# Performance work log

Hardware: AMD Instinct MI355X
Metric: run time of the kernel (lower is better)

## Reference

```python
import jax, jax.numpy as jnp
import numpy as np

N_FEATURES = 128
N_ACTIONS = 16
HIDDEN = 256
BATCH = 4096
IN_DIM = N_FEATURES + N_ACTIONS  # 144


def setup_inputs() -> dict:
    key = jax.random.key(0)
    k1, k2, k3, k4 = jax.random.split(key, 4)
    f_t = jax.random.normal(k1, (BATCH, N_FEATURES), dtype=jnp.float32)
    a_t = jax.random.normal(k2, (BATCH, N_ACTIONS), dtype=jnp.float32)
    # Stacked per-feature MLP params (one small MLP per output feature).
    W1 = jax.random.normal(k3, (N_FEATURES, IN_DIM, HIDDEN), dtype=jnp.float32) / np.sqrt(IN_DIM)
    b1 = jnp.zeros((N_FEATURES, HIDDEN), dtype=jnp.float32)
    W2 = jax.random.normal(k4, (N_FEATURES, HIDDEN), dtype=jnp.float32) / np.sqrt(HIDDEN)
    b2 = jnp.zeros((N_FEATURES,), dtype=jnp.float32)
    return {"f_t": f_t, "a_t": a_t, "W1": W1, "b1": b1, "W2": W2, "b2": b2}


def reference(f_t, a_t, W1, b1, W2, b2):
    # fa_t: [B, F+A] shared input to all per-feature models
    fa_t = jnp.concatenate((f_t, a_t), axis=1)
    # Grouped GEMM replacing parallel_apply over n_features tiny MLPs:
    # h: [M, B, H]
    h = jax.nn.relu(jnp.einsum('bi,mih->mbh', fa_t, W1) + b1[:, None, :])
    # out: [B, M]  (each model emits a single scalar per example)
    out = jnp.einsum('mbh,mh->bm', h, W2) + b2[None, :]
    # skip_connection=True, additional=False, all=False -> add f_t
    return out + f_t
```

## Files before the change

### kernel.cpp

```cpp
#include <hip/hip_runtime.h>
#include <hip/hip_bf16.h>

#define BATCH   4096
#define NF      128
#define NA      16
#define IN_DIM  144
#define KP      144
#define KF      192
#define HID     256

typedef __attribute__((ext_vector_type(8))) short bf16x8;
typedef __attribute__((ext_vector_type(4))) float f32x4;
typedef __attribute__((ext_vector_type(16))) float f32x16;
typedef unsigned int u32;

__device__ __forceinline__ void gl_lds16(const void* gsrc, void* ldst) {
    __builtin_amdgcn_global_load_lds(
        (const __attribute__((address_space(1))) u32*)gsrc,
        (__attribute__((address_space(3))) u32*)ldst, 16, 0, 0);
}

__device__ __host__ __forceinline__ int swzkey(int row) {
    return (row + (row >> 3)) & 7;
}

__global__ void convert_all(const float* __restrict__ W1,
                            const float* __restrict__ f_t,
                            const float* __restrict__ a_t,
                            __hip_bfloat16* __restrict__ w1t,
                            __hip_bfloat16* __restrict__ fab) {
    const int bid = blockIdx.x;
    const int t = threadIdx.x;
    if (bid < 1152) {
        __shared__ float tile[16][HID];
        int m = bid / 9;
        int kc = bid - m * 9;
        int k0 = kc * 16;
#pragma unroll
        for (int i = 0; i < 16; ++i)
            tile[i][t] = W1[((size_t)m * IN_DIM + (k0 + i)) * HID + t];
        __syncthreads();
        union { ushort us[16]; uint4 q[2]; } pk;
#pragma unroll
        for (int i = 0; i < 16; ++i) {
            __hip_bfloat16 h = __float2bfloat16(tile[i][t]);
            pk.us[i] = *(ushort*)&h;
        }
        uint4* dst = (uint4*)(w1t + ((size_t)m * HID + t) * KP + k0);
        dst[0] = pk.q[0];
        dst[1] = pk.q[1];
    } else {
        int c = (bid - 1152) * 256 + t;
        const int total = BATCH * (KF / 8);
        if (c >= total) return;
        int row = c / 24;
        int cc = c - row * 24;
        union { ushort us[8]; uint4 q; } pk;
#pragma unroll
        for (int j = 0; j < 8; ++j) {
            int k = cc * 8 + j;
            float v;
            if (k < NF)            v = f_t[(size_t)row * NF + k];
            else if (k < IN_DIM)   v = a_t[(size_t)row * NA + (k - NF)];
            else                   v = 0.0f;
            __hip_bfloat16 h = __float2bfloat16(v);
            pk.us[j] = *(ushort*)&h;
        }
        int pc = cc ^ swzkey(row);
        *(uint4*)(fab + (size_t)row * KF + pc * 8) = pk.q;
    }
}

__global__ __launch_bounds__(256, 2) void fused_mlp(
        const __hip_bfloat16* __restrict__ fab,
        const __hip_bfloat16* __restrict__ w1t,
        const float* __restrict__ b1,
        const float* __restrict__ W2,
        const float* __restrict__ b2,
        const float* __restrict__ f_t,
        float* __restrict__ out) {
    __shared__ __align__(16) __hip_bfloat16 Abuf[2][64 * KF];
    __shared__ __align__(16) float partial[2][4][64];

    const int bid = blockIdx.x;
    const int m     = bid & 127;
    const int slice = bid >> 7;
    const int row_base = slice * 1024;
    const int t = threadIdx.x;
    const int w = t >> 6;
    const int lane = t & 63;
    const int l31 = lane & 31;
    const int h = lane >> 5;
    const int x0 = swzkey(l31) << 4;
    const int x1 = ((swzkey(l31) + 4) & 7) << 4;

    bf16x8 bfrag[2][9];
#pragma unroll
    for (int hi2 = 0; hi2 < 2; ++hi2) {
        const int col = w * 64 + hi2 * 32 + l31;
        const __hip_bfloat16* wp = w1t + ((size_t)m * HID + col) * KP + h * 8;
#pragma unroll
        for (int ks = 0; ks < 9; ++ks)
            bfrag[hi2][ks] = *(const bf16x8*)(wp + ks * 16);
    }
    f32x16 w2v[2], b1v[2];
#pragma unroll
    for (int hi2 = 0; hi2 < 2; ++hi2) {
        const float* wp2 = W2 + (size_t)m * HID + w * 64 + hi2 * 32 + 4 * h;
        const float* bp1 = b1 + (size_t)m * HID + w * 64 + hi2 * 32 + 4 * h;
#pragma unroll
        for (int q = 0; q < 4; ++q) {
            f32x4 v = *(const f32x4*)(wp2 + 8 * q);
            f32x4 bv = *(const f32x4*)(bp1 + 8 * q);
#pragma unroll
            for (int i = 0; i < 4; ++i) {
                w2v[hi2][q * 4 + i] = v[i];
                b1v[hi2][q * 4 + i] = bv[i];
            }
        }
    }
    const float b2v = b2[m];

    {
        const char* src = (const char*)(fab + (size_t)row_base * KF);
        char* dst = (char*)&Abuf[0][0];
#pragma unroll
        for (int i = 0; i < 6; ++i)
            gl_lds16(src + (size_t)(t + i * 256) * 16, dst + (t + i * 256) * 16);
    }
    __syncthreads();

    for (int tile = 0; tile < 16; ++tile) {
        const int cur = tile & 1;
        const int r0 = row_base + tile * 64;

        if (tile < 15) {
            const char* src = (const char*)(fab + (size_t)(r0 + 64) * KF);
            char* dst = (char*)&Abuf[cur ^ 1][0];
#pragma unroll
            for (int i = 0; i < 6; ++i)
                gl_lds16(src + (size_t)(t + i * 256) * 16, dst + (t + i * 256) * 16);
        }
        float skipv = 0.0f;
        if (t < 64) skipv = f_t[(size_t)(r0 + t) * NF + m];

        f32x16 acc[2][2];
        const char* ab = (const char*)&Abuf[cur][0];

        {
            bf16x8 a[2];
            a[0] = *(const bf16x8*)(ab + l31 * 384 + ((h * 16) ^ x0));
            a[1] = *(const bf16x8*)(ab + (32 + l31) * 384 + ((h * 16) ^ x1));
#pragma unroll
            for (int hi2 = 0; hi2 < 2; ++hi2)
#pragma unroll
                for (int bj2 = 0; bj2 < 2; ++bj2)
                    acc[hi2][bj2] = __builtin_amdgcn_mfma_f32_32x32x16_bf16(
                        bfrag[hi2][0], a[bj2], b1v[hi2], 0, 0, 0);
        }
#pragma unroll
        for (int ks = 1; ks < 9; ++ks) {
            bf16x8 a[2];
            int cb = ks * 32 + h * 16;
            a[0] = *(const bf16x8*)(ab + l31 * 384 + (cb ^ x0));
            a[1] = *(const bf16x8*)(ab + (32 + l31) * 384 + (cb ^ x1));
#pragma unroll
            for (int hi2 = 0; hi2 < 2; ++hi2)
#pragma unroll
                for (int bj2 = 0; bj2 < 2; ++bj2)
                    acc[hi2][bj2] = __builtin_amdgcn_mfma_f32_32x32x16_bf16(
                        bfrag[hi2][ks], a[bj2], acc[hi2][bj2], 0, 0, 0);
        }

        float sarr[2];
#pragma unroll
        for (int bj2 = 0; bj2 < 2; ++bj2) {
            float sr0 = 0.f, sr1 = 0.f, sr2 = 0.f, sr3 = 0.f;
#pragma unroll
            for (int hi2 = 0; hi2 < 2; ++hi2)
#pragma unroll
                for (int q = 0; q < 4; ++q) {
                    float h0 = acc[hi2][bj2][q*4+0]; h0 = h0 > 0.f ? h0 : 0.f;
                    float h1 = acc[hi2][bj2][q*4+1]; h1 = h1 > 0.f ? h1 : 0.f;
                    float h2 = acc[hi2][bj2][q*4+2]; h2 = h2 > 0.f ? h2 : 0.f;
                    float h3 = acc[hi2][bj2][q*4+3]; h3 = h3 > 0.f ? h3 : 0.f;
                    sr0 = fmaf(h0, w2v[hi2][q*4+0], sr0);
                    sr1 = fmaf(h1, w2v[hi2][q*4+1], sr1);
                    sr2 = fmaf(h2, w2v[hi2][q*4+2], sr2);
                    sr3 = fmaf(h3, w2v[hi2][q*4+3], sr3);
                }
            float s = (sr0 + sr1) + (sr2 + sr3);
            s += __shfl_xor(s, 32, 64);
            sarr[bj2] = s;
        }
        if (h == 0) {
            partial[cur][w][l31]      = sarr[0];
            partial[cur][w][32 + l31] = sarr[1];
        }

        __syncthreads();
        if (t < 64) {
            float v = (partial[cur][0][t] + partial[cur][1][t])
                    + (partial[cur][2][t] + partial[cur][3][t])
                    + b2v + skipv;
            out[(size_t)(r0 + t) * NF + m] = v;
        }
    }
}

extern "C" void kernel_launch(void* const* d_in, const int* in_sizes, int n_in,
                              void* d_out, int out_size, void* d_ws, size_t ws_size,
                              hipStream_t stream) {
    const float* f_t = (const float*)d_in[0];
    const float* a_t = (const float*)d_in[1];
    const float* W1  = (const float*)d_in[2];
    const float* b1  = (const float*)d_in[3];
    const float* W2  = (const float*)d_in[4];
    const float* b2  = (const float*)d_in[5];
    float* out = (float*)d_out;

    __hip_bfloat16* w1t = (__hip_bfloat16*)d_ws;
    __hip_bfloat16* fab = (__hip_bfloat16*)((char*)d_ws + (size_t)NF * HID * KP * 2);

    hipLaunchKernelGGL(convert_all, dim3(1536), dim3(256), 0, stream,
                       W1, f_t, a_t, w1t, fab);
    hipLaunchKernelGGL(fused_mlp, dim3(512), dim3(256), 0, stream,
                       fab, w1t, b1, W2, b2, f_t, out);
}
```

Measured before the change: 56.69 us.

## Load activations directly from global in MFMA-fragment layout, drop LDS staging

The activation matrix is now written by the conversion kernel in a chunked layout of 8-element k-chunks by batch row, so each lane can load its MFMA A-fragment directly from global memory. This removes the swizzled LDS double buffer, the global-to-LDS copies and the per-tile __syncthreads. Partial sums for all 16 tiles are kept in LDS and reduced once at the end, with the output writes and skip-add spread across all threads. In exchange, every k-step now waits on global/L2 latency with no explicit prefetch, and the padding in the activation buffer is removed.

```diff
diff --git a/kernel.cpp b/kernel.cpp
--- a/kernel.cpp
+++ b/kernel.cpp
@@ -6,29 +6,18 @@
 #define NA      16
 #define IN_DIM  144
 #define KP      144
-#define KF      192
+#define NKC     18
 #define HID     256
 
 typedef __attribute__((ext_vector_type(8))) short bf16x8;
 typedef __attribute__((ext_vector_type(4))) float f32x4;
 typedef __attribute__((ext_vector_type(16))) float f32x16;
-typedef unsigned int u32;
-
-__device__ __forceinline__ void gl_lds16(const void* gsrc, void* ldst) {
-    __builtin_amdgcn_global_load_lds(
-        (const __attribute__((address_space(1))) u32*)gsrc,
-        (__attribute__((address_space(3))) u32*)ldst, 16, 0, 0);
-}
-
-__device__ __host__ __forceinline__ int swzkey(int row) {
-    return (row + (row >> 3)) & 7;
-}
 
 __global__ void convert_all(const float* __restrict__ W1,
                             const float* __restrict__ f_t,
                             const float* __restrict__ a_t,
                             __hip_bfloat16* __restrict__ w1t,
-                            __hip_bfloat16* __restrict__ fab) {
+                            __hip_bfloat16* __restrict__ fab2) {
     const int bid = blockIdx.x;
     const int t = threadIdx.x;
     if (bid < 1152) {
@@ -50,37 +39,31 @@
         dst[0] = pk.q[0];
         dst[1] = pk.q[1];
     } else {
-        int c = (bid - 1152) * 256 + t;
-        const int total = BATCH * (KF / 8);
-        if (c >= total) return;
-        int row = c / 24;
-        int cc = c - row * 24;
+        int b2i = bid - 1152;
+        int cc = b2i / 16;
+        int rb = b2i - cc * 16;
+        int row = rb * 256 + t;
         union { ushort us[8]; uint4 q; } pk;
+        const float* src = (cc < 16) ? (f_t + (size_t)row * NF + cc * 8)
+                                     : (a_t + (size_t)row * NA + (cc - 16) * 8);
 #pragma unroll
         for (int j = 0; j < 8; ++j) {
-            int k = cc * 8 + j;
-            float v;
-            if (k < NF)            v = f_t[(size_t)row * NF + k];
-            else if (k < IN_DIM)   v = a_t[(size_t)row * NA + (k - NF)];
-            else                   v = 0.0f;
-            __hip_bfloat16 h = __float2bfloat16(v);
+            __hip_bfloat16 h = __float2bfloat16(src[j]);
             pk.us[j] = *(ushort*)&h;
         }
-        int pc = cc ^ swzkey(row);
-        *(uint4*)(fab + (size_t)row * KF + pc * 8) = pk.q;
+        *(uint4*)(fab2 + ((size_t)cc * BATCH + row) * 8) = pk.q;
     }
 }
 
 __global__ __launch_bounds__(256, 2) void fused_mlp(
-        const __hip_bfloat16* __restrict__ fab,
+        const __hip_bfloat16* __restrict__ fab2,
         const __hip_bfloat16* __restrict__ w1t,
         const float* __restrict__ b1,
         const float* __restrict__ W2,
         const float* __restrict__ b2,
         const float* __restrict__ f_t,
         float* __restrict__ out) {
-    __shared__ __align__(16) __hip_bfloat16 Abuf[2][64 * KF];
-    __shared__ __align__(16) float partial[2][4][64];
+    __shared__ __align__(16) float partial[16][4][64];
 
     const int bid = blockIdx.x;
     const int m     = bid & 127;
@@ -91,8 +74,6 @@
     const int lane = t & 63;
     const int l31 = lane & 31;
     const int h = lane >> 5;
-    const int x0 = swzkey(l31) << 4;
-    const int x1 = ((swzkey(l31) + 4) & 7) << 4;
 
     bf16x8 bfrag[2][9];
 #pragma unroll
@@ -121,55 +102,35 @@
     }
     const float b2v = b2[m];
 
-    {
-        const char* src = (const char*)(fab + (size_t)row_base * KF);
-        char* dst = (char*)&Abuf[0][0];
-#pragma unroll
-        for (int i = 0; i < 6; ++i)
-            gl_lds16(src + (size_t)(t + i * 256) * 16, dst + (t + i * 256) * 16);
-    }
-    __syncthreads();
-
     for (int tile = 0; tile < 16; ++tile) {
-        const int cur = tile & 1;
         const int r0 = row_base + tile * 64;
-
-        if (tile < 15) {
-            const char* src = (const char*)(fab + (size_t)(r0 + 64) * KF);
-            char* dst = (char*)&Abuf[cur ^ 1][0];
-#pragma unroll
-            for (int i = 0; i < 6; ++i)
-                gl_lds16(src + (size_t)(t + i * 256) * 16, dst + (t + i * 256) * 16);
-        }
-        float skipv = 0.0f;
-        if (t < 64) skipv = f_t[(size_t)(r0 + t) * NF + m];
+        const __hip_bfloat16* fb0 = fab2 + ((size_t)h * BATCH + r0 + l31) * 8;
+        const __hip_bfloat16* fb1 = fb0 + 32 * 8;
 
         f32x16 acc[2][2];
-        const char* ab = (const char*)&Abuf[cur][0];
 
         {
-            bf16x8 a[2];
-            a[0] = *(const bf16x8*)(ab + l31 * 384 + ((h * 16) ^ x0));
-            a[1] = *(const bf16x8*)(ab + (32 + l31) * 384 + ((h * 16) ^ x1));
+            bf16x8 a0 = *(const bf16x8*)fb0;
+            bf16x8 a1 = *(const bf16x8*)fb1;
 #pragma unroll
-            for (int hi2 = 0; hi2 < 2; ++hi2)
-#pragma unroll
-                for (int bj2 = 0; bj2 < 2; ++bj2)
-                    acc[hi2][bj2] = __builtin_amdgcn_mfma_f32_32x32x16_bf16(
-                        bfrag[hi2][0], a[bj2], b1v[hi2], 0, 0, 0);
+            for (int hi2 = 0; hi2 < 2; ++hi2) {
+                acc[hi2][0] = __builtin_amdgcn_mfma_f32_32x32x16_bf16(
+                    bfrag[hi2][0], a0, b1v[hi2], 0, 0, 0);
+                acc[hi2][1] = __builtin_amdgcn_mfma_f32_32x32x16_bf16(
+                    bfrag[hi2][0], a1, b1v[hi2], 0, 0, 0);
+            }
         }
 #pragma unroll
         for (int ks = 1; ks < 9; ++ks) {
-            bf16x8 a[2];
-            int cb = ks * 32 + h * 16;
-            a[0] = *(const bf16x8*)(ab + l31 * 384 + (cb ^ x0));
-            a[1] = *(const bf16x8*)(ab + (32 + l31) * 384 + (cb ^ x1));
+            bf16x8 a0 = *(const bf16x8*)(fb0 + (size_t)ks * 2 * BATCH * 8);
+            bf16x8 a1 = *(const bf16x8*)(fb1 + (size_t)ks * 2 * BATCH * 8);
 #pragma unroll
-            for (int hi2 = 0; hi2 < 2; ++hi2)
-#pragma unroll
-                for (int bj2 = 0; bj2 < 2; ++bj2)
-                    acc[hi2][bj2] = __builtin_amdgcn_mfma_f32_32x32x16_bf16(
-                        bfrag[hi2][ks], a[bj2], acc[hi2][bj2], 0, 0, 0);
+            for (int hi2 = 0; hi2 < 2; ++hi2) {
+                acc[hi2][0] = __builtin_amdgcn_mfma_f32_32x32x16_bf16(
+                    bfrag[hi2][ks], a0, acc[hi2][0], 0, 0, 0);
+                acc[hi2][1] = __builtin_amdgcn_mfma_f32_32x32x16_bf16(
+                    bfrag[hi2][ks], a1, acc[hi2][1], 0, 0, 0);
+            }
         }
 
         float sarr[2];
@@ -194,17 +155,22 @@
             sarr[bj2] = s;
         }
         if (h == 0) {
-            partial[cur][w][l31]      = sarr[0];
-            partial[cur][w][32 + l31] = sarr[1];
+            partial[tile][w][l31]      = sarr[0];
+            partial[tile][w][32 + l31] = sarr[1];
         }
+    }
 
-        __syncthreads();
-        if (t < 64) {
-            float v = (partial[cur][0][t] + partial[cur][1][t])
-                    + (partial[cur][2][t] + partial[cur][3][t])
-                    + b2v + skipv;
-            out[(size_t)(r0 + t) * NF + m] = v;
-        }
+    __syncthreads();
+#pragma unroll
+    for (int i = 0; i < 4; ++i) {
+        int idx = i * 256 + t;
+        int tl = idx >> 6;
+        int r  = idx & 63;
+        int row = row_base + tl * 64 + r;
+        float v = (partial[tl][0][r] + partial[tl][1][r])
+                + (partial[tl][2][r] + partial[tl][3][r])
+                + b2v + f_t[(size_t)row * NF + m];
+        out[(size_t)row * NF + m] = v;
     }
 }
 
@@ -219,11 +185,11 @@
     const float* b2  = (const float*)d_in[5];
     float* out = (float*)d_out;
 
-    __hip_bfloat16* w1t = (__hip_bfloat16*)d_ws;
-    __hip_bfloat16* fab = (__hip_bfloat16*)((char*)d_ws + (size_t)NF * HID * KP * 2);
+    __hip_bfloat16* w1t  = (__hip_bfloat16*)d_ws;
+    __hip_bfloat16* fab2 = (__hip_bfloat16*)((char*)d_ws + (size_t)NF * HID * KP * 2);
 
-    hipLaunchKernelGGL(convert_all, dim3(1536), dim3(256), 0, stream,
-                       W1, f_t, a_t, w1t, fab);
+    hipLaunchKernelGGL(convert_all, dim3(1440), dim3(256), 0, stream,
+                       W1, f_t, a_t, w1t, fab2);
     hipLaunchKernelGGL(fused_mlp, dim3(512), dim3(256), 0, stream,
-                       fab, w1t, b1, W2, b2, f_t, out);
+                       fab2, w1t, b1, W2, b2, f_t, out);
 }
```

Measured after the change: 59.72 us. +5.3%, slower.

## Store activations chunk-major per tile, drop K padding, and double the grid

Applied to the files above, without the earlier changes.

Activations are now written in a chunk-major layout per 64-row tile (18 chunks of 8 bf16) instead of padded row-major 192-wide rows with an XOR swizzle. This removes the zero-padding to 192 columns and makes LDS fragment reads contiguous without swizzle arithmetic. Each block now handles 512 rows instead of 1024, so the grid doubles to 1024 blocks for better occupancy and load balance. The cost is more redundant loading of per-model weight fragments into registers, since twice as many blocks each load them.

```diff
diff --git a/kernel.cpp b/kernel.cpp
--- a/kernel.cpp
+++ b/kernel.cpp
@@ -6,7 +6,7 @@
 #define NA      16
 #define IN_DIM  144
 #define KP      144
-#define KF      192
+#define NCH     18
 #define HID     256
 
 typedef __attribute__((ext_vector_type(8))) short bf16x8;
@@ -20,15 +20,11 @@
         (__attribute__((address_space(3))) u32*)ldst, 16, 0, 0);
 }
 
-__device__ __host__ __forceinline__ int swzkey(int row) {
-    return (row + (row >> 3)) & 7;
-}
-
 __global__ void convert_all(const float* __restrict__ W1,
                             const float* __restrict__ f_t,
                             const float* __restrict__ a_t,
                             __hip_bfloat16* __restrict__ w1t,
-                            __hip_bfloat16* __restrict__ fab) {
+                            __hip_bfloat16* __restrict__ fabT) {
     const int bid = blockIdx.x;
     const int t = threadIdx.x;
     if (bid < 1152) {
@@ -50,49 +46,46 @@
         dst[0] = pk.q[0];
         dst[1] = pk.q[1];
     } else {
-        int c = (bid - 1152) * 256 + t;
-        const int total = BATCH * (KF / 8);
-        if (c >= total) return;
-        int row = c / 24;
-        int cc = c - row * 24;
+        int o = (bid - 1152) * 256 + t;
+        const int total = (BATCH / 64) * NCH * 64;
+        if (o >= total) return;
+        int r  = o & 63;
+        int cc = (o >> 6) % NCH;
+        int T  = o / (NCH * 64);
+        int row = T * 64 + r;
         union { ushort us[8]; uint4 q; } pk;
+        const float* src = (cc < 16) ? (f_t + (size_t)row * NF + cc * 8)
+                                     : (a_t + (size_t)row * NA + (cc - 16) * 8);
 #pragma unroll
         for (int j = 0; j < 8; ++j) {
-            int k = cc * 8 + j;
-            float v;
-            if (k < NF)            v = f_t[(size_t)row * NF + k];
-            else if (k < IN_DIM)   v = a_t[(size_t)row * NA + (k - NF)];
-            else                   v = 0.0f;
-            __hip_bfloat16 h = __float2bfloat16(v);
+            __hip_bfloat16 h = __float2bfloat16(src[j]);
             pk.us[j] = *(ushort*)&h;
         }
-        int pc = cc ^ swzkey(row);
-        *(uint4*)(fab + (size_t)row * KF + pc * 8) = pk.q;
+        *(uint4*)(fabT + (size_t)o * 8) = pk.q;
     }
 }
 
 __global__ __launch_bounds__(256, 2) void fused_mlp(
-        const __hip_bfloat16* __restrict__ fab,
+        const __hip_bfloat16* __restrict__ fabT,
         const __hip_bfloat16* __restrict__ w1t,
         const float* __restrict__ b1,
         const float* __restrict__ W2,
         const float* __restrict__ b2,
         const float* __restrict__ f_t,
         float* __restrict__ out) {
-    __shared__ __align__(16) __hip_bfloat16 Abuf[2][64 * KF];
+    __shared__ __align__(16) __hip_bfloat16 Abuf[2][NCH * 64 * 8];
     __shared__ __align__(16) float partial[2][4][64];
 
     const int bid = blockIdx.x;
     const int m     = bid & 127;
     const int slice = bid >> 7;
-    const int row_base = slice * 1024;
+    const int row_base = slice * 512;
+    const int T0 = row_base / 64;
     const int t = threadIdx.x;
     const int w = t >> 6;
     const int lane = t & 63;
     const int l31 = lane & 31;
     const int h = lane >> 5;
-    const int x0 = swzkey(l31) << 4;
-    const int x1 = ((swzkey(l31) + 4) & 7) << 4;
 
     bf16x8 bfrag[2][9];
 #pragma unroll
@@ -121,26 +114,27 @@
     }
     const float b2v = b2[m];
 
-    {
-        const char* src = (const char*)(fab + (size_t)row_base * KF);
-        char* dst = (char*)&Abuf[0][0];
-#pragma unroll
-        for (int i = 0; i < 6; ++i)
-            gl_lds16(src + (size_t)(t + i * 256) * 16, dst + (t + i * 256) * 16);
-    }
+#define STAGE(BUF, TG)                                                        \
+    {                                                                         \
+        const char* src = (const char*)fabT + (size_t)(TG) * (NCH * 64 * 16); \
+        char* dst = (char*)&Abuf[BUF][0];                                     \
+        _Pragma("unroll")                                                     \
+        for (int i = 0; i < 4; ++i)                                           \
+            gl_lds16(src + (size_t)(t + i * 256) * 16,                        \
+                     dst + (t + i * 256) * 16);                               \
+        if (t < 128)                                                          \
+            gl_lds16(src + (size_t)(1024 + t) * 16, dst + (1024 + t) * 16);   \
+    }
+
+    STAGE(0, T0);
     __syncthreads();
 
-    for (int tile = 0; tile < 16; ++tile) {
+    for (int tile = 0; tile < 8; ++tile) {
         const int cur = tile & 1;
         const int r0 = row_base + tile * 64;
 
-        if (tile < 15) {
-            const char* src = (const char*)(fab + (size_t)(r0 + 64) * KF);
-            char* dst = (char*)&Abuf[cur ^ 1][0];
-#pragma unroll
-            for (int i = 0; i < 6; ++i)
-                gl_lds16(src + (size_t)(t + i * 256) * 16, dst + (t + i * 256) * 16);
-        }
+        if (tile < 7) STAGE(cur ^ 1, T0 + tile + 1);
+
         float skipv = 0.0f;
         if (t < 64) skipv = f_t[(size_t)(r0 + t) * NF + m];
 
@@ -149,8 +143,8 @@
 
         {
             bf16x8 a[2];
-            a[0] = *(const bf16x8*)(ab + l31 * 384 + ((h * 16) ^ x0));
-            a[1] = *(const bf16x8*)(ab + (32 + l31) * 384 + ((h * 16) ^ x1));
+            a[0] = *(const bf16x8*)(ab + (h * 64 + l31) * 16);
+            a[1] = *(const bf16x8*)(ab + (h * 64 + 32 + l31) * 16);
 #pragma unroll
             for (int hi2 = 0; hi2 < 2; ++hi2)
 #pragma unroll
@@ -161,9 +155,9 @@
 #pragma unroll
         for (int ks = 1; ks < 9; ++ks) {
             bf16x8 a[2];
-            int cb = ks * 32 + h * 16;
-            a[0] = *(const bf16x8*)(ab + l31 * 384 + (cb ^ x0));
-            a[1] = *(const bf16x8*)(ab + (32 + l31) * 384 + (cb ^ x1));
+            const int cb = (2 * ks + h) * 64;
+            a[0] = *(const bf16x8*)(ab + (cb + l31) * 16);
+            a[1] = *(const bf16x8*)(ab + (cb + 32 + l31) * 16);
 #pragma unroll
             for (int hi2 = 0; hi2 < 2; ++hi2)
 #pragma unroll
@@ -206,6 +200,7 @@
             out[(size_t)(r0 + t) * NF + m] = v;
         }
     }
+#undef STAGE
 }
 
 extern "C" void kernel_launch(void* const* d_in, const int* in_sizes, int n_in,
@@ -219,11 +214,11 @@
     const float* b2  = (const float*)d_in[5];
     float* out = (float*)d_out;
 
-    __hip_bfloat16* w1t = (__hip_bfloat16*)d_ws;
-    __hip_bfloat16* fab = (__hip_bfloat16*)((char*)d_ws + (size_t)NF * HID * KP * 2);
-
-    hipLaunchKernelGGL(convert_all, dim3(1536), dim3(256), 0, stream,
-                       W1, f_t, a_t, w1t, fab);
-    hipLaunchKernelGGL(fused_mlp, dim3(512), dim3(256), 0, stream,
-                       fab, w1t, b1, W2, b2, f_t, out);
-}
+    __hip_bfloat16* w1t  = (__hip_bfloat16*)d_ws;
+    __hip_bfloat16* fabT = (__hip_bfloat16*)((char*)d_ws + (size_t)NF * HID * KP * 2);
+
+    hipLaunchKernelGGL(convert_all, dim3(1440), dim3(256), 0, stream,
+                       W1, f_t, a_t, w1t, fabT);
+    hipLaunchKernelGGL(fused_mlp, dim3(1024), dim3(256), 0, stream,
+                       fabT, w1t, b1, W2, b2, f_t, out);
+}
```

Result: faster. 55.02 us (-2.9%).
